# Kernel optimization log

Measured on AMD Instinct MI355X. Metric: run time of the kernel, lower is better.

## Reference

```python
import math
import jax, jax.numpy as jnp
import numpy as np
from jax import lax

MUL = 16          # multiplicity of 0e and 1o in irreps_in/out
NB = 4            # num_radial_basis
DIAM = 5.0        # kernel diameter (mm)
R = DIAM / 2.0
STEP_MM = 1.0     # isotropic voxel step


def _lattice_constants():
    """Constant lattice, spherical harmonics (component norm) and radial embedding."""
    s = int(math.floor(R / STEP_MM))                       # 2 -> side 5
    c = np.arange(-s, s + 1.0) * STEP_MM
    lat = np.stack(np.meshgrid(c, c, c, indexing='ij'), axis=-1)   # [5,5,5,3]
    norm = np.linalg.norm(lat, axis=-1)                    # [5,5,5]
    safe = np.where(norm == 0.0, 1.0, norm)
    nvec = np.where(norm[..., None] > 0.0, lat / safe[..., None], 0.0)
    sh1 = np.sqrt(3.0) * nvec                              # l=1 SH, component norm; 0 at origin
    # soft_one_hot_linspace, basis='smooth_finite', start_zero=end_zero=True
    values = np.linspace(0.0, R, NB + 2)[1:-1]             # [NB]
    step = R / (NB + 1)
    d = (norm[..., None] - values) / step                  # [5,5,5,NB]
    dd = np.clip(d, -1.0 + 1e-9, 1.0 - 1e-9)
    emb = np.where(np.abs(d) < 1.0,
                   1.14136 * np.e ** 2 * np.exp(-1.0 / (1.0 - dd ** 2)), 0.0)
    nlat = float(lat.shape[0] * lat.shape[1] * lat.shape[2])
    return (jnp.asarray(sh1, jnp.float32), jnp.asarray(emb, jnp.float32), nlat)

_SH1, _EMB, _NLAT = _lattice_constants()


def _build_kernel(w000, w011, w101, w110, sc0, sc1):
    """Radial basis x Clebsch-Gordan kernel build. Returns [5,5,5,64,64] (XYZIO)."""
    # per-path spatially varying radial weights [x,y,z,u,w]
    r000 = jnp.einsum('xyzb,buw->xyzuw', _EMB, w000) / _NLAT
    r011 = jnp.einsum('xyzb,buw->xyzuw', _EMB, w011) / _NLAT
    r101 = jnp.einsum('xyzb,buw->xyzuw', _EMB, w101) / _NLAT
    r110 = jnp.einsum('xyzb,buw->xyzuw', _EMB, w110) / _NLAT
    X, Y, Z = _EMB.shape[:3]
    eye3 = jnp.eye(3, dtype=w000.dtype)
    # CG (orthonormal per output component):
    # 0e x 0e -> 0e : C = 1
    k00 = r000                                                        # [...,16,16]
    # 0e x 1o -> 1o : C[j,k] = delta
    k01 = jnp.einsum('xyzuw,xyzk->xyzuwk', r011, _SH1).reshape(X, Y, Z, MUL, 3 * MUL)
    # 1o x 0e -> 1o : C[i,k] = delta (sh0 component = 1 everywhere)
    k11 = jnp.einsum('xyzuw,ik->xyzuiwk', r101, eye3).reshape(X, Y, Z, 3 * MUL, 3 * MUL)
    # 1o x 1o -> 0e : C[i,j] = delta/sqrt(3)
    k10 = jnp.einsum('xyzuw,xyzi->xyzuiw', r110, _SH1).reshape(X, Y, Z, 3 * MUL, MUL) / jnp.sqrt(3.0)
    top = jnp.concatenate([k00, k01], axis=-1)   # [...,16,64]
    bot = jnp.concatenate([k10, k11], axis=-1)   # [...,48,64]
    k = jnp.concatenate([top, bot], axis=-2)     # [...,64,64]
    # self-connection overwrites the center tap (FunctionalLinear, std 1/sqrt(mul))
    lin00 = sc0 / jnp.sqrt(float(MUL))
    lin11 = jnp.einsum('uw,ik->uiwk', sc1 / jnp.sqrt(float(MUL)), eye3).reshape(3 * MUL, 3 * MUL)
    z16 = jnp.zeros((MUL, 3 * MUL), dtype=w000.dtype)
    lin = jnp.concatenate([
        jnp.concatenate([lin00, z16], axis=1),
        jnp.concatenate([z16.T, lin11], axis=1)], axis=0)             # [64,64]
    k = k.at[X // 2, Y // 2, Z // 2].set(lin)
    return k


def setup_inputs() -> dict:
    key = jax.random.key(0)
    ks = jax.random.split(key, 7)
    std_tp = 1.0 / math.sqrt(2 * MUL)   # fan-in: 2 paths x mul=16 per output irrep
    std_sc = 1.0 / math.sqrt(MUL)
    return {
        'x': jax.random.normal(ks[0], (2, 48, 48, 48, 4 * MUL), jnp.float32),
        'w000': std_tp * jax.random.normal(ks[1], (NB, MUL, MUL), jnp.float32),
        'w011': std_tp * jax.random.normal(ks[2], (NB, MUL, MUL), jnp.float32),
        'w101': std_tp * jax.random.normal(ks[3], (NB, MUL, MUL), jnp.float32),
        'w110': std_tp * jax.random.normal(ks[4], (NB, MUL, MUL), jnp.float32),
        'sc0': std_sc * jax.random.normal(ks[5], (MUL, MUL), jnp.float32),
        'sc1': std_sc * jax.random.normal(ks[6], (MUL, MUL), jnp.float32),
    }


def reference(x, w000, w011, w101, w110, sc0, sc1):
    k = _build_kernel(w000, w011, w101, w110, sc0, sc1)
    return lax.conv_general_dilated(
        lhs=x, rhs=k, window_strides=(1, 1, 1), padding='SAME',
        dimension_numbers=('NXYZC', 'XYZIO', 'NXYZC'))
```

## Files before the change

kernel.cpp:

```cpp
#include <hip/hip_runtime.h>
#include <math.h>

typedef __attribute__((ext_vector_type(8))) short short8;
typedef __attribute__((ext_vector_type(4))) float float4v;

#define NS 48
#define PS 52
#define NC 64

__device__ __align__(16) unsigned short g_xb[(size_t)2 * PS * PS * PS * NC];
__device__ __align__(16) unsigned short g_kb[125 * 2 * 4 * 64 * 8];

__device__ __forceinline__ unsigned short bf16r(float f) {
  unsigned u = __builtin_bit_cast(unsigned, f);
  u = (u + 0x7FFFu + ((u >> 16) & 1u)) >> 16;
  return (unsigned short)u;
}

__global__ __launch_bounds__(256) void pad_cast(const float* __restrict__ x) {
  const int bx = blockIdx.x;
  const int n = blockIdx.y;
  const int xx = bx / 52, yy = bx % 52;
  const bool inxy = (xx >= 2) && (xx < 50) && (yy >= 2) && (yy < 50);
  unsigned short* dst = g_xb + (((size_t)n * 52 + xx) * 52 + yy) * 3328;
  const float* src = x + ((((size_t)n * 48 + (xx - 2)) * 48 + (yy - 2)) * 48) * 64;
#pragma unroll 1
  for (int tt = threadIdx.x; tt < 832; tt += 256) {
    const int zz = tt >> 4;
    const int i4 = (tt & 15) * 4;
    ushort4 v = make_ushort4(0, 0, 0, 0);
    if (inxy && zz >= 2 && zz < 50) {
      const float4 f = *(const float4*)(src + (size_t)(zz - 2) * 64 + i4);
      v.x = bf16r(f.x); v.y = bf16r(f.y); v.z = bf16r(f.z); v.w = bf16r(f.w);
    }
    *(ushort4*)(dst + (size_t)zz * 64 + i4) = v;
  }
}

__global__ __launch_bounds__(256) void build_kb(
    const float* __restrict__ w000, const float* __restrict__ w011,
    const float* __restrict__ w101, const float* __restrict__ w110,
    const float* __restrict__ sc0,  const float* __restrict__ sc1) {
  const int tap = blockIdx.x;
  const int tz = tap % 5, ty = (tap / 5) % 5, tx = tap / 25;
  const float cx = (float)(tx - 2), cy = (float)(ty - 2), cz = (float)(tz - 2);
  const float norm = sqrtf(cx * cx + cy * cy + cz * cz);
  const float inv = (norm > 0.f) ? (1.f / norm) : 0.f;
  const float SQ3 = 1.7320508075688772f;
  const float sh[3] = {SQ3 * cx * inv, SQ3 * cy * inv, SQ3 * cz * inv};
  float emb[4];
#pragma unroll
  for (int b = 0; b < 4; ++b) {
    const float v = 0.5f * (float)(b + 1);
    const float d = (norm - v) * 2.0f;
    emb[b] = (fabsf(d) < 1.f) ? 1.14136f * expf(2.f - 1.f / (1.f - d * d)) : 0.f;
  }
  const bool center = (tap == 62);
  const float INV_NLAT = 1.0f / 125.0f;
  const float INV_SQ3 = 0.57735026918962576f;
  for (int e = threadIdx.x; e < 4096; e += blockDim.x) {
    const int r = e >> 6, c = e & 63;
    float val = 0.f;
    if (center) {
      if (r < 16 && c < 16) {
        val = sc0[r * 16 + c] * 0.25f;
      } else if (r >= 16 && c >= 16) {
        const int u = (r - 16) / 3, i = (r - 16) % 3;
        const int w = (c - 16) / 3, kc = (c - 16) % 3;
        val = (i == kc) ? sc1[u * 16 + w] * 0.25f : 0.f;
      }
    } else {
      if (r < 16 && c < 16) {
        float a = 0.f;
#pragma unroll
        for (int b = 0; b < 4; ++b) a += emb[b] * w000[(b * 16 + r) * 16 + c];
        val = a * INV_NLAT;
      } else if (r < 16) {
        const int w = (c - 16) / 3, kc = (c - 16) % 3;
        float a = 0.f;
#pragma unroll
        for (int b = 0; b < 4; ++b) a += emb[b] * w011[(b * 16 + r) * 16 + w];
        val = a * INV_NLAT * sh[kc];
      } else if (c < 16) {
        const int u = (r - 16) / 3, i = (r - 16) % 3;
        float a = 0.f;
#pragma unroll
        for (int b = 0; b < 4; ++b) a += emb[b] * w110[(b * 16 + u) * 16 + c];
        val = a * INV_NLAT * sh[i] * INV_SQ3;
      } else {
        const int u = (r - 16) / 3, i = (r - 16) % 3;
        const int w = (c - 16) / 3, kc = (c - 16) % 3;
        if (i == kc) {
          float a = 0.f;
#pragma unroll
          for (int b = 0; b < 4; ++b) a += emb[b] * w101[(b * 16 + u) * 16 + w];
          val = a * INV_NLAT;
        }
      }
    }
    const int ik = r >> 5;
    const int lane = ((r >> 3) & 3) * 16 + (c & 15);
    const int of = c >> 4;
    const int j = r & 7;
    g_kb[((size_t)((tap * 2 + ik) * 4 + of) * 64 + lane) * 8 + j] = bf16r(val);
  }
}

__global__ __launch_bounds__(256, 3) void conv_mfma(float* __restrict__ out) {
  __shared__ __align__(16) char xs[12 * 52 * 64];
  const int t = threadIdx.x;
  const int l = t & 63;
  const int wid = t >> 6;
  const int m = l & 15;
  const int kq = l >> 4;
  const int bid = blockIdx.x;
  const int wg = (bid & 7) * 72 + (bid >> 3);
  const int X = wg % 48;
  const int yg = (wg / 48) % 6;
  const int n = wg / 288;
  const int y0 = yg << 3;

  float4v acc[2][3][4];
  const float4v zero4 = {0.f, 0.f, 0.f, 0.f};
#pragma unroll
  for (int y = 0; y < 2; ++y)
#pragma unroll
    for (int zt = 0; zt < 3; ++zt)
#pragma unroll
      for (int of = 0; of < 4; ++of) acc[y][zt][of] = zero4;

#pragma unroll 1
  for (int dx = 0; dx < 5; ++dx) {
    const unsigned short* gx =
        g_xb + ((size_t)n * PS + (X + dx)) * 173056 + (size_t)y0 * 3328;
#pragma unroll 1
    for (int h = 0; h < 2; ++h) {
      __syncthreads();
#pragma unroll
      for (int s = 0; s < 10; ++s) {
        const int cl = t + (s << 8);
        if (cl < 2496) {
          const int ry = cl >> 2, p = cl & 3;
          const int jy = ry / 52, zz = ry - jy * 52;
          const int sc = p ^ ((ry >> 1) & 3);
          const unsigned short* g = gx + jy * 3328 + zz * 64 + h * 32 + sc * 8;
          char* ldsd = xs + (size_t)((t >> 6) * 64 + (s << 8)) * 16;
          __builtin_amdgcn_global_load_lds(
              (const __attribute__((address_space(1))) unsigned*)g,
              (__attribute__((address_space(3))) unsigned*)ldsd, 16, 0, 0);
        }
      }
      __syncthreads();

#pragma unroll 1
      for (int dy = 0; dy < 5; ++dy) {
        const int rbase = (2 * wid + dy) * 52 + m;
        const int tapb = ((dx * 5 + dy) * 5) * 2 + h;
#pragma unroll
        for (int dz = 0; dz < 5; ++dz) {
          const unsigned short* kbp =
              g_kb + (size_t)(tapb + dz * 2) * 2048 + l * 8;
          const short8 b0 = *(const short8*)(kbp);
          const short8 b1 = *(const short8*)(kbp + 512);
          const short8 b2 = *(const short8*)(kbp + 1024);
          const short8 b3 = *(const short8*)(kbp + 1536);
          short8 a[2][3];
#pragma unroll
          for (int y = 0; y < 2; ++y) {
#pragma unroll
            for (int zt = 0; zt < 3; ++zt) {
              const int ry = rbase + y * 52 + zt * 16 + dz;
              const int byte = ry * 64 + ((kq ^ ((ry >> 1) & 3)) << 4);
              a[y][zt] = *(const short8*)(xs + byte);
            }
          }
#pragma unroll
          for (int y = 0; y < 2; ++y) {
#pragma unroll
            for (int zt = 0; zt < 3; ++zt) {
              acc[y][zt][0] = __builtin_amdgcn_mfma_f32_16x16x32_bf16(a[y][zt], b0, acc[y][zt][0], 0, 0, 0);
              acc[y][zt][1] = __builtin_amdgcn_mfma_f32_16x16x32_bf16(a[y][zt], b1, acc[y][zt][1], 0, 0, 0);
              acc[y][zt][2] = __builtin_amdgcn_mfma_f32_16x16x32_bf16(a[y][zt], b2, acc[y][zt][2], 0, 0, 0);
              acc[y][zt][3] = __builtin_amdgcn_mfma_f32_16x16x32_bf16(a[y][zt], b3, acc[y][zt][3], 0, 0, 0);
            }
          }
        }
      }
    }
  }

#pragma unroll
  for (int y = 0; y < 2; ++y) {
    float* op = out +
        ((((size_t)n * NS + X) * NS + (y0 + 2 * wid + y)) * NS) * NC;
#pragma unroll
    for (int zt = 0; zt < 3; ++zt) {
#pragma unroll
      for (int of = 0; of < 4; ++of) {
#pragma unroll
        for (int r = 0; r < 4; ++r) {
          const int z = zt * 16 + kq * 4 + r;
          const int o = of * 16 + m;
          op[(size_t)z * NC + o] = acc[y][zt][of][r];
        }
      }
    }
  }
}

extern "C" void kernel_launch(void* const* d_in, const int* in_sizes, int n_in,
                              void* d_out, int out_size, void* d_ws, size_t ws_size,
                              hipStream_t stream) {
  const float* x    = (const float*)d_in[0];
  const float* w000 = (const float*)d_in[1];
  const float* w011 = (const float*)d_in[2];
  const float* w101 = (const float*)d_in[3];
  const float* w110 = (const float*)d_in[4];
  const float* sc0  = (const float*)d_in[5];
  const float* sc1  = (const float*)d_in[6];
  float* out = (float*)d_out;

  pad_cast<<<dim3(52 * 52, 2), 256, 0, stream>>>(x);
  build_kb<<<125, 256, 0, stream>>>(w000, w011, w101, w110, sc0, sc1);
  conv_mfma<<<576, 256, 0, stream>>>(out);
}
```

Before: 251.3 us.

## Fully unroll the dy/dz tap loop with precomputed swizzled LDS offsets and setprio

Merges the dx/h loops into a single phase loop and fully unrolls all 25 dy×dz taps per phase. The swizzled LDS read addresses come from eight precomputed per-lane offsets, so the unrolled body uses constant offsets instead of recomputing XOR swizzles. MFMA blocks are wrapped in s_setprio to favour matrix issue across waves. Launch bounds drop from 3 to 2 blocks per SM, which allows more registers for the unrolled code but lowers occupancy.

```diff
diff --git a/kernel.cpp b/kernel.cpp
--- a/kernel.cpp
+++ b/kernel.cpp
@@ -106,7 +106,7 @@
   }
 }
 
-__global__ __launch_bounds__(256, 3) void conv_mfma(float* __restrict__ out) {
+__global__ __launch_bounds__(256, 2) void conv_mfma(float* __restrict__ out) {
   __shared__ __align__(16) char xs[12 * 52 * 64];
   const int t = threadIdx.x;
   const int l = t & 63;
@@ -120,6 +120,13 @@
   const int n = wg / 288;
   const int y0 = yg << 3;
 
+  unsigned a8[8];
+#pragma unroll
+  for (int p = 0; p < 8; ++p) {
+    const int r0 = 104 * wid + p + m;
+    a8[p] = (unsigned)(r0 * 64 + ((kq ^ ((r0 >> 1) & 3)) << 4));
+  }
+
   float4v acc[2][3][4];
   const float4v zero4 = {0.f, 0.f, 0.f, 0.f};
 #pragma unroll
@@ -130,12 +137,12 @@
       for (int of = 0; of < 4; ++of) acc[y][zt][of] = zero4;
 
 #pragma unroll 1
-  for (int dx = 0; dx < 5; ++dx) {
-    const unsigned short* gx =
-        g_xb + ((size_t)n * PS + (X + dx)) * 173056 + (size_t)y0 * 3328;
-#pragma unroll 1
-    for (int h = 0; h < 2; ++h) {
-      __syncthreads();
+  for (int ph = 0; ph < 10; ++ph) {
+    const int dx = ph >> 1, h = ph & 1;
+    __syncthreads();
+    {
+      const unsigned short* gx =
+          g_xb + ((size_t)n * PS + (X + dx)) * 173056 + (size_t)y0 * 3328;
 #pragma unroll
       for (int s = 0; s < 10; ++s) {
         const int cl = t + (s << 8);
@@ -144,48 +151,45 @@
           const int jy = ry / 52, zz = ry - jy * 52;
           const int sc = p ^ ((ry >> 1) & 3);
           const unsigned short* g = gx + jy * 3328 + zz * 64 + h * 32 + sc * 8;
-          char* ldsd = xs + (size_t)((t >> 6) * 64 + (s << 8)) * 16;
+          char* ldsd = xs + (size_t)(((t >> 6) * 64 + (s << 8)) * 16);
           __builtin_amdgcn_global_load_lds(
               (const __attribute__((address_space(1))) unsigned*)g,
               (__attribute__((address_space(3))) unsigned*)ldsd, 16, 0, 0);
         }
       }
-      __syncthreads();
-
-#pragma unroll 1
-      for (int dy = 0; dy < 5; ++dy) {
-        const int rbase = (2 * wid + dy) * 52 + m;
-        const int tapb = ((dx * 5 + dy) * 5) * 2 + h;
-#pragma unroll
-        for (int dz = 0; dz < 5; ++dz) {
-          const unsigned short* kbp =
-              g_kb + (size_t)(tapb + dz * 2) * 2048 + l * 8;
-          const short8 b0 = *(const short8*)(kbp);
-          const short8 b1 = *(const short8*)(kbp + 512);
-          const short8 b2 = *(const short8*)(kbp + 1024);
-          const short8 b3 = *(const short8*)(kbp + 1536);
-          short8 a[2][3];
-#pragma unroll
-          for (int y = 0; y < 2; ++y) {
-#pragma unroll
-            for (int zt = 0; zt < 3; ++zt) {
-              const int ry = rbase + y * 52 + zt * 16 + dz;
-              const int byte = ry * 64 + ((kq ^ ((ry >> 1) & 3)) << 4);
-              a[y][zt] = *(const short8*)(xs + byte);
-            }
-          }
-#pragma unroll
-          for (int y = 0; y < 2; ++y) {
-#pragma unroll
-            for (int zt = 0; zt < 3; ++zt) {
-              acc[y][zt][0] = __builtin_amdgcn_mfma_f32_16x16x32_bf16(a[y][zt], b0, acc[y][zt][0], 0, 0, 0);
-              acc[y][zt][1] = __builtin_amdgcn_mfma_f32_16x16x32_bf16(a[y][zt], b1, acc[y][zt][1], 0, 0, 0);
-              acc[y][zt][2] = __builtin_amdgcn_mfma_f32_16x16x32_bf16(a[y][zt], b2, acc[y][zt][2], 0, 0, 0);
-              acc[y][zt][3] = __builtin_amdgcn_mfma_f32_16x16x32_bf16(a[y][zt], b3, acc[y][zt][3], 0, 0, 0);
-            }
-          }
-        }
-      }
+    }
+    __syncthreads();
+
+    const unsigned short* kb0 = g_kb + (size_t)(dx * 50 + h) * 2048 + l * 8;
+
+#pragma unroll
+    for (int g = 0; g < 25; ++g) {
+      const int dy_ = g / 5, dz_ = g % 5;
+      const unsigned short* kbp = kb0 + (size_t)g * 4096;
+      const short8 b0 = *(const short8*)(kbp);
+      const short8 b1 = *(const short8*)(kbp + 512);
+      const short8 b2 = *(const short8*)(kbp + 1024);
+      const short8 b3 = *(const short8*)(kbp + 1536);
+      short8 a[2][3];
+#pragma unroll
+      for (int y = 0; y < 2; ++y)
+#pragma unroll
+        for (int zt = 0; zt < 3; ++zt) {
+          const int K = (dy_ + y) * 52 + zt * 16 + dz_;
+          a[y][zt] = *(const short8*)(
+              xs + a8[K & 7] + (unsigned)((K - (K & 7)) * 64));
+        }
+      __builtin_amdgcn_s_setprio(1);
+#pragma unroll
+      for (int y = 0; y < 2; ++y)
+#pragma unroll
+        for (int zt = 0; zt < 3; ++zt) {
+          acc[y][zt][0] = __builtin_amdgcn_mfma_f32_16x16x32_bf16(a[y][zt], b0, acc[y][zt][0], 0, 0, 0);
+          acc[y][zt][1] = __builtin_amdgcn_mfma_f32_16x16x32_bf16(a[y][zt], b1, acc[y][zt][1], 0, 0, 0);
+          acc[y][zt][2] = __builtin_amdgcn_mfma_f32_16x16x32_bf16(a[y][zt], b2, acc[y][zt][2], 0, 0, 0);
+          acc[y][zt][3] = __builtin_amdgcn_mfma_f32_16x16x32_bf16(a[y][zt], b3, acc[y][zt][3], 0, 0, 0);
+        }
+      __builtin_amdgcn_s_setprio(0);
     }
   }
 
```

New measurement: 275.3 us. 9.6% more time.
